# Performance work log

Measured on AMD Instinct MI355X. Metric: run time of the kernel, lower is better.

Reference implementation:

```python
import jax, jax.numpy as jnp
import numpy as np

E = 8                 # n_experts
CAPACITY_FACTOR = 1.25

B, T, H, I = 4, 1024, 2048, 1408


def setup_inputs() -> dict:
    key = jax.random.key(0)
    k0, k1, k2, k3, k4 = jax.random.split(key, 5)
    x = jax.random.normal(k0, (B, T, H), jnp.float32)
    Wr = jax.random.normal(k1, (E, H), jnp.float32) * 0.02   # router proj (no bias)
    Wg = jax.random.normal(k2, (E, I, H), jnp.float32) * 0.02  # gate_proj per expert
    Wu = jax.random.normal(k3, (E, I, H), jnp.float32) * 0.02  # up_proj per expert
    Wd = jax.random.normal(k4, (E, H, I), jnp.float32) * 0.02  # down_proj per expert
    return {"x": x, "Wr": Wr, "Wg": Wg, "Wu": Wu, "Wd": Wd}


def reference(x, Wr, Wg, Wu, Wd):
    Bb, Tt, Hh = x.shape
    N = Bb * Tt
    cap = max(1, int(CAPACITY_FACTOR * (N * 2 / E)))
    xf = x.reshape(N, Hh)

    # --- Top2Router (noise_std=0 -> no noise) ---
    logits = jnp.einsum('nh,eh->ne', xf, Wr)          # [N, E]
    gate = jax.nn.softmax(logits, axis=-1)
    top2_val, top2_idx = jax.lax.top_k(gate, 2)        # [N, 2]

    # --- capacity masking, matching torch loop order: slot k=0 over all
    # tokens (flat order), then slot k=1; within an expert the first `cap`
    # assignments are kept ---
    flat_idx = jnp.concatenate([top2_idx[:, 0], top2_idx[:, 1]])   # [2N]
    flat_val = jnp.concatenate([top2_val[:, 0], top2_val[:, 1]])   # [2N]
    onehot = jax.nn.one_hot(flat_idx, E, dtype=jnp.int32)          # [2N, E]
    rank = (jnp.cumsum(onehot, axis=0) * onehot).sum(-1)           # inclusive rank within expert
    keep = rank <= cap                                             # [2N]
    w_assign = jnp.where(keep, flat_val, 0.0)

    # combine weights per (token, expert); top-2 experts per token are distinct
    tok = jnp.tile(jnp.arange(N), 2)
    comb = jnp.zeros((N, E), x.dtype).at[tok, flat_idx].add(w_assign)  # [N, E]

    # --- per-expert SwiGLU FFN applied densely, combined with gate weights ---
    g = jax.nn.silu(jnp.einsum('nh,eih->eni', xf, Wg))  # [E, N, I]
    u = jnp.einsum('nh,eih->eni', xf, Wu)               # [E, N, I]
    out_e = jnp.einsum('eni,ehi->enh', g * u, Wd)       # [E, N, H]
    y = jnp.einsum('ne,enh->nh', comb, out_e)           # [N, H]
    return y.reshape(Bb, Tt, Hh)
```

## Files before the change

### kernel.cpp

```cpp
#include <hip/hip_runtime.h>
#include <hip/hip_bf16.h>

#define N_TOK 4096
#define H_DIM 2048
#define I_DIM 1408
#define E_NUM 8
#define CAP   1280

typedef __hip_bfloat16 bf16;
typedef unsigned short us;
typedef __bf16 bf16x8 __attribute__((ext_vector_type(8)));
typedef float f32x4 __attribute__((ext_vector_type(4)));

__device__ inline void gld_lds16(const void* g, void* l) {
    __builtin_amdgcn_global_load_lds((const __attribute__((address_space(1))) void*)g,
                                     (__attribute__((address_space(3))) void*)l,
                                     16, 0, 0);
}

__device__ inline void cvt_body8(const float* __restrict__ s, us* __restrict__ d, long i, long n) {
    if (i >= n) return;
    float4 v0 = *(const float4*)(s + i);
    float4 v1 = *(const float4*)(s + i + 4);
    union { us u[8]; uint4 q; } o;
    float f[8] = {v0.x, v0.y, v0.z, v0.w, v1.x, v1.y, v1.z, v1.w};
#pragma unroll
    for (int j = 0; j < 8; j++) {
        bf16 b = __float2bfloat16(f[j]);
        o.u[j] = *(us*)&b;
    }
    *(uint4*)(d + i) = o.q;
}

__global__ void cvt8(const float* __restrict__ s, us* __restrict__ d, long n) {
    long i = ((long)blockIdx.x * blockDim.x + threadIdx.x) * 8;
    cvt_body8(s, d, i, n);
}

__global__ void cvt_w3(const float* __restrict__ s0, const float* __restrict__ s1,
                       const float* __restrict__ s2, us* __restrict__ d0,
                       us* __restrict__ d1, us* __restrict__ d2, long n) {
    long i = ((long)blockIdx.x * blockDim.x + threadIdx.x) * 8;
    const float* s = blockIdx.z == 0 ? s0 : (blockIdx.z == 1 ? s1 : s2);
    us* d = blockIdx.z == 0 ? d0 : (blockIdx.z == 1 ? d1 : d2);
    cvt_body8(s, d, i, n);
}

__global__ void router_k(const float* __restrict__ x, const float* __restrict__ Wr,
                         float* __restrict__ top_val, int* __restrict__ top_idx) {
    int tok  = (blockIdx.x * blockDim.x + threadIdx.x) >> 6;
    int lane = threadIdx.x & 63;
    if (tok >= N_TOK) return;
    const float* xr = x + (size_t)tok * H_DIM;
    float acc[E_NUM];
#pragma unroll
    for (int e = 0; e < E_NUM; e++) acc[e] = 0.f;
    for (int h = lane; h < H_DIM; h += 64) {
        float xv = xr[h];
#pragma unroll
        for (int e = 0; e < E_NUM; e++) acc[e] += xv * Wr[e * H_DIM + h];
    }
#pragma unroll
    for (int e = 0; e < E_NUM; e++) {
#pragma unroll
        for (int off = 32; off > 0; off >>= 1) acc[e] += __shfl_xor(acc[e], off, 64);
    }
    if (lane == 0) {
        float mx = acc[0];
#pragma unroll
        for (int e = 1; e < E_NUM; e++) mx = fmaxf(mx, acc[e]);
        float p[E_NUM], s = 0.f;
#pragma unroll
        for (int e = 0; e < E_NUM; e++) { p[e] = __expf(acc[e] - mx); s += p[e]; }
        float inv = 1.f / s;
#pragma unroll
        for (int e = 0; e < E_NUM; e++) p[e] *= inv;
        int i0 = 0;
#pragma unroll
        for (int e = 1; e < E_NUM; e++) if (p[e] > p[i0]) i0 = e;
        int i1 = -1;
#pragma unroll
        for (int e = 0; e < E_NUM; e++) {
            if (e == i0) continue;
            if (i1 < 0 || p[e] > p[i1]) i1 = e;
        }
        top_idx[tok * 2]     = i0;
        top_idx[tok * 2 + 1] = i1;
        top_val[tok * 2]     = p[i0];
        top_val[tok * 2 + 1] = p[i1];
    }
}

__global__ void assign_k(const int* __restrict__ top_idx, const float* __restrict__ top_val,
                         int* __restrict__ toklist, int* __restrict__ pos,
                         float* __restrict__ wz, int* __restrict__ counts) {
    const int T = 256;
    const int CH = (2 * N_TOK) / T;
    int t = threadIdx.x;
    for (int i = t; i < E_NUM * CAP; i += T) toklist[i] = N_TOK;
    __shared__ int cnt[T][E_NUM];
    int local[E_NUM];
#pragma unroll
    for (int e = 0; e < E_NUM; e++) local[e] = 0;
    for (int q = 0; q < CH; q++) {
        int j = t * CH + q;
        int slot = j >> 12;
        int tok  = j & 4095;
        int e = top_idx[tok * 2 + slot];
        local[e]++;
    }
#pragma unroll
    for (int e = 0; e < E_NUM; e++) cnt[t][e] = local[e];
    __syncthreads();
    if (t < E_NUM) {
        int run = 0;
        for (int i = 0; i < T; i++) { int c = cnt[i][t]; cnt[i][t] = run; run += c; }
        counts[t] = run < CAP ? run : CAP;
    }
    __syncthreads();
    int run[E_NUM];
#pragma unroll
    for (int e = 0; e < E_NUM; e++) run[e] = cnt[t][e];
    for (int q = 0; q < CH; q++) {
        int j = t * CH + q;
        int slot = j >> 12;
        int tok  = j & 4095;
        int e = top_idx[tok * 2 + slot];
        int rank = ++run[e];
        if (rank <= CAP) {
            toklist[e * CAP + rank - 1] = tok;
            pos[tok * 2 + slot] = e * CAP + rank - 1;
            wz[tok * 2 + slot]  = top_val[tok * 2 + slot];
        } else {
            pos[tok * 2 + slot] = -1;
            wz[tok * 2 + slot]  = 0.f;
        }
    }
}

__global__ __launch_bounds__(256, 2)
void gu_fused(const us* __restrict__ A, const us* __restrict__ Wg,
              const us* __restrict__ Wu, us* __restrict__ hbuf,
              const int* __restrict__ toklist, const int* __restrict__ counts) {
    const int e  = blockIdx.z;
    const int m0 = blockIdx.x * 128;
    const int n0 = blockIdx.y * 128;
    if (m0 >= counts[e]) return;

    __shared__ us As[128 * 64];
    __shared__ us Bg[128 * 64];
    __shared__ us Bu[128 * 64];

    const int t  = threadIdx.x;
    const int r0 = t >> 2;
    const int c8 = (t & 3) * 8;

    int tok0 = toklist[e * CAP + m0 + r0];
    int tok1 = toklist[e * CAP + m0 + r0 + 64];
    const us* aP0 = A + (size_t)tok0 * H_DIM + c8;
    const us* aP1 = A + (size_t)tok1 * H_DIM + c8;
    const us* gP0 = Wg + ((size_t)e * I_DIM + n0 + r0) * H_DIM + c8;
    const us* gP1 = gP0 + (size_t)64 * H_DIM;
    const us* uP0 = Wu + ((size_t)e * I_DIM + n0 + r0) * H_DIM + c8;
    const us* uP1 = uP0 + (size_t)64 * H_DIM;

    us* lA0 = As + t * 8;  us* lA1 = lA0 + 64 * 32;
    us* lG0 = Bg + t * 8;  us* lG1 = lG0 + 64 * 32;
    us* lU0 = Bu + t * 8;  us* lU1 = lU0 + 64 * 32;

    const int lane = t & 63;
    const int wave = t >> 6;
    const int wm   = (wave & 1) * 64;
    const int wn   = (wave >> 1) * 64;
    const int l15  = lane & 15;
    const int quad = lane >> 4;

    f32x4 ag[4][4], au[4][4];
#pragma unroll
    for (int i = 0; i < 4; i++)
#pragma unroll
        for (int j = 0; j < 4; j++) {
            ag[i][j] = (f32x4){0.f, 0.f, 0.f, 0.f};
            au[i][j] = (f32x4){0.f, 0.f, 0.f, 0.f};
        }

    for (int k = 0; k < H_DIM; k += 64) {
        gld_lds16(aP0,      lA0);
        gld_lds16(aP1,      lA1);
        gld_lds16(aP0 + 32, lA0 + 4096);
        gld_lds16(aP1 + 32, lA1 + 4096);
        gld_lds16(gP0,      lG0);
        gld_lds16(gP1,      lG1);
        gld_lds16(gP0 + 32, lG0 + 4096);
        gld_lds16(gP1 + 32, lG1 + 4096);
        gld_lds16(uP0,      lU0);
        gld_lds16(uP1,      lU1);
        gld_lds16(uP0 + 32, lU0 + 4096);
        gld_lds16(uP1 + 32, lU1 + 4096);
        aP0 += 64; aP1 += 64; gP0 += 64; gP1 += 64; uP0 += 64; uP1 += 64;
        __syncthreads();
#pragma unroll
        for (int kk = 0; kk < 2; kk++) {
            bf16x8 af[4];
#pragma unroll
            for (int i = 0; i < 4; i++)
                af[i] = *(const bf16x8*)(As + kk * 4096 + (wm + i * 16 + l15) * 32 + quad * 8);
            {
                bf16x8 bfr[4];
#pragma unroll
                for (int j = 0; j < 4; j++)
                    bfr[j] = *(const bf16x8*)(Bg + kk * 4096 + (wn + j * 16 + l15) * 32 + quad * 8);
#pragma unroll
                for (int i = 0; i < 4; i++)
#pragma unroll
                    for (int j = 0; j < 4; j++)
                        ag[i][j] = __builtin_amdgcn_mfma_f32_16x16x32_bf16(af[i], bfr[j], ag[i][j], 0, 0, 0);
            }
            {
                bf16x8 bfr[4];
#pragma unroll
                for (int j = 0; j < 4; j++)
                    bfr[j] = *(const bf16x8*)(Bu + kk * 4096 + (wn + j * 16 + l15) * 32 + quad * 8);
#pragma unroll
                for (int i = 0; i < 4; i++)
#pragma unroll
                    for (int j = 0; j < 4; j++)
                        au[i][j] = __builtin_amdgcn_mfma_f32_16x16x32_bf16(af[i], bfr[j], au[i][j], 0, 0, 0);
            }
        }
        __syncthreads();
    }

#pragma unroll
    for (int i = 0; i < 4; i++) {
        int mb = m0 + wm + i * 16 + quad * 4;
#pragma unroll
        for (int r = 0; r < 4; r++) {
            size_t rowoff = ((size_t)e * CAP + mb + r) * I_DIM;
#pragma unroll
            for (int j = 0; j < 4; j++) {
                int n = n0 + wn + j * 16 + l15;
                float g = ag[i][j][r];
                g = g / (1.f + __expf(-g));
                float hv = g * au[i][j][r];
                bf16 b = __float2bfloat16(hv);
                hbuf[rowoff + n] = *(us*)&b;
            }
        }
    }
}

__global__ __launch_bounds__(256, 3)
void down_gemm(const us* __restrict__ A, const us* __restrict__ W,
               float* __restrict__ dbuf, const int* __restrict__ counts) {
    const int e  = blockIdx.z;
    const int m0 = blockIdx.x * 128;
    const int n0 = blockIdx.y * 128;
    if (m0 >= counts[e]) return;

    __shared__ us As[128 * 64];
    __shared__ us Bs[128 * 64];

    const int t  = threadIdx.x;
    const int r0 = t >> 2;
    const int c8 = (t & 3) * 8;

    const us* aP0 = A + ((size_t)e * CAP + m0 + r0) * (size_t)I_DIM + c8;
    const us* aP1 = aP0 + (size_t)64 * I_DIM;
    const us* bP0 = W + ((size_t)e * H_DIM + n0 + r0) * (size_t)I_DIM + c8;
    const us* bP1 = bP0 + (size_t)64 * I_DIM;

    us* lA0 = As + t * 8;  us* lA1 = lA0 + 64 * 32;
    us* lB0 = Bs + t * 8;  us* lB1 = lB0 + 64 * 32;

    const int lane = t & 63;
    const int wave = t >> 6;
    const int wm   = (wave & 1) * 64;
    const int wn   = (wave >> 1) * 64;
    const int l15  = lane & 15;
    const int quad = lane >> 4;

    f32x4 acc[4][4];
#pragma unroll
    for (int i = 0; i < 4; i++)
#pragma unroll
        for (int j = 0; j < 4; j++) acc[i][j] = (f32x4){0.f, 0.f, 0.f, 0.f};

    for (int k = 0; k < I_DIM; k += 64) {
        gld_lds16(aP0,      lA0);
        gld_lds16(aP1,      lA1);
        gld_lds16(aP0 + 32, lA0 + 4096);
        gld_lds16(aP1 + 32, lA1 + 4096);
        gld_lds16(bP0,      lB0);
        gld_lds16(bP1,      lB1);
        gld_lds16(bP0 + 32, lB0 + 4096);
        gld_lds16(bP1 + 32, lB1 + 4096);
        aP0 += 64; aP1 += 64; bP0 += 64; bP1 += 64;
        __syncthreads();
#pragma unroll
        for (int kk = 0; kk < 2; kk++) {
            bf16x8 af[4], bfr[4];
#pragma unroll
            for (int i = 0; i < 4; i++)
                af[i] = *(const bf16x8*)(As + kk * 4096 + (wm + i * 16 + l15) * 32 + quad * 8);
#pragma unroll
            for (int j = 0; j < 4; j++)
                bfr[j] = *(const bf16x8*)(Bs + kk * 4096 + (wn + j * 16 + l15) * 32 + quad * 8);
#pragma unroll
            for (int i = 0; i < 4; i++)
#pragma unroll
                for (int j = 0; j < 4; j++)
                    acc[i][j] = __builtin_amdgcn_mfma_f32_16x16x32_bf16(af[i], bfr[j], acc[i][j], 0, 0, 0);
        }
        __syncthreads();
    }

#pragma unroll
    for (int i = 0; i < 4; i++) {
        int mb = m0 + wm + i * 16 + quad * 4;
#pragma unroll
        for (int r = 0; r < 4; r++) {
            float* orow = dbuf + ((size_t)e * CAP + mb + r) * H_DIM + n0 + wn + l15;
#pragma unroll
            for (int j = 0; j < 4; j++)
                orow[j * 16] = acc[i][j][r];
        }
    }
}

__global__ void combine_k(const float* __restrict__ dbuf, const int* __restrict__ pos,
                          const float* __restrict__ wz, float* __restrict__ out) {
    int tok = blockIdx.x;
    int off = threadIdx.x * 8;
    int p0 = pos[tok * 2], p1 = pos[tok * 2 + 1];
    float w0 = wz[tok * 2], w1 = wz[tok * 2 + 1];
    float4 z = {0.f, 0.f, 0.f, 0.f};
    float4 a0 = z, a1 = z, b0 = z, b1 = z;
    if (p0 >= 0) {
        const float* r = dbuf + (size_t)p0 * H_DIM + off;
        a0 = *(const float4*)r; a1 = *(const float4*)(r + 4);
    }
    if (p1 >= 0) {
        const float* r = dbuf + (size_t)p1 * H_DIM + off;
        b0 = *(const float4*)r; b1 = *(const float4*)(r + 4);
    }
    float4 o0, o1;
    o0.x = w0 * a0.x + w1 * b0.x;  o0.y = w0 * a0.y + w1 * b0.y;
    o0.z = w0 * a0.z + w1 * b0.z;  o0.w = w0 * a0.w + w1 * b0.w;
    o1.x = w0 * a1.x + w1 * b1.x;  o1.y = w0 * a1.y + w1 * b1.y;
    o1.z = w0 * a1.z + w1 * b1.z;  o1.w = w0 * a1.w + w1 * b1.w;
    float* orow = out + (size_t)tok * H_DIM + off;
    *(float4*)orow = o0;
    *(float4*)(orow + 4) = o1;
}

extern "C" void kernel_launch(void* const* d_in, const int* in_sizes, int n_in,
                              void* d_out, int out_size, void* d_ws, size_t ws_size,
                              hipStream_t stream) {
    const float* x  = (const float*)d_in[0];
    const float* Wr = (const float*)d_in[1];
    const float* Wg = (const float*)d_in[2];
    const float* Wu = (const float*)d_in[3];
    const float* Wd = (const float*)d_in[4];
    float* out = (float*)d_out;

    char* p = (char*)d_ws;
    auto alloc = [&](size_t bytes) { char* r = p; p += (bytes + 255) & ~(size_t)255; return r; };
    us* xb   = (us*)alloc((size_t)(N_TOK + 1) * H_DIM * 2);
    us* Wgb  = (us*)alloc((size_t)E_NUM * I_DIM * H_DIM * 2);
    us* Wub  = (us*)alloc((size_t)E_NUM * I_DIM * H_DIM * 2);
    us* Wdb  = (us*)alloc((size_t)E_NUM * H_DIM * I_DIM * 2);
    us* hbuf = (us*)alloc((size_t)E_NUM * CAP * I_DIM * 2);
    float* top_val = (float*)alloc((size_t)N_TOK * 2 * 4);
    int*   top_idx = (int*)alloc((size_t)N_TOK * 2 * 4);
    int*   toklist = (int*)alloc((size_t)E_NUM * CAP * 4);
    int*   posm    = (int*)alloc((size_t)N_TOK * 2 * 4);
    float* wz      = (float*)alloc((size_t)N_TOK * 2 * 4);
    int*   counts  = (int*)alloc((size_t)E_NUM * 4);
    float* dbuf = (float*)Wgb;

    hipMemsetAsync(xb + (size_t)N_TOK * H_DIM, 0, H_DIM * 2, stream);

    long nx = (long)N_TOK * H_DIM;
    long nw = (long)E_NUM * I_DIM * H_DIM;
    cvt8<<<dim3((unsigned)((nx / 8 + 255) / 256)), dim3(256), 0, stream>>>(x, xb, nx);
    cvt_w3<<<dim3((unsigned)((nw / 8 + 255) / 256), 1, 3), dim3(256), 0, stream>>>(
        Wg, Wu, Wd, Wgb, Wub, Wdb, nw);

    router_k<<<dim3(N_TOK / 4), dim3(256), 0, stream>>>(x, Wr, top_val, top_idx);
    assign_k<<<dim3(1), dim3(256), 0, stream>>>(top_idx, top_val, toklist, posm, wz, counts);

    dim3 g1(CAP / 128, I_DIM / 128, E_NUM);
    gu_fused<<<g1, dim3(256), 0, stream>>>(xb, Wgb, Wub, hbuf, toklist, counts);

    dim3 g2(CAP / 128, H_DIM / 128, E_NUM);
    down_gemm<<<g2, dim3(256), 0, stream>>>(hbuf, Wdb, dbuf, counts);

    combine_k<<<dim3(N_TOK), dim3(256), 0, stream>>>(dbuf, posm, wz, out);
}
```

Measured before the change: 607.5 us.

## Fuse fp32-to-bf16 weight conversion into the expert GEMM tile loaders

Drops the separate pass that converts the gate, up and down weights to bf16 in workspace. The GEMM kernels now read fp32 weights directly and convert them to bf16 in registers before storing into LDS. This removes a full read-and-write pass over roughly 280 MB of weights. In exchange, the weight loads become ordinary synchronous loads instead of async global-to-LDS copies, and every M-tile re-reads twice as many bytes of weights. dbuf also gets its own workspace allocation instead of reusing the converted-weight buffer.

```diff
diff --git a/kernel.cpp b/kernel.cpp
--- a/kernel.cpp
+++ b/kernel.cpp
@@ -18,7 +18,21 @@
                                      16, 0, 0);
 }
 
-__device__ inline void cvt_body8(const float* __restrict__ s, us* __restrict__ d, long i, long n) {
+__device__ inline void stage_f32(const float* __restrict__ src, us* dst) {
+    float4 a = *(const float4*)src;
+    float4 b = *(const float4*)(src + 4);
+    union { us u[8]; uint4 q; } o;
+    float f[8] = {a.x, a.y, a.z, a.w, b.x, b.y, b.z, b.w};
+#pragma unroll
+    for (int j = 0; j < 8; j++) {
+        bf16 v = __float2bfloat16(f[j]);
+        o.u[j] = *(us*)&v;
+    }
+    *(uint4*)dst = o.q;
+}
+
+__global__ void cvt8(const float* __restrict__ s, us* __restrict__ d, long n) {
+    long i = ((long)blockIdx.x * blockDim.x + threadIdx.x) * 8;
     if (i >= n) return;
     float4 v0 = *(const float4*)(s + i);
     float4 v1 = *(const float4*)(s + i + 4);
@@ -30,20 +44,6 @@
         o.u[j] = *(us*)&b;
     }
     *(uint4*)(d + i) = o.q;
-}
-
-__global__ void cvt8(const float* __restrict__ s, us* __restrict__ d, long n) {
-    long i = ((long)blockIdx.x * blockDim.x + threadIdx.x) * 8;
-    cvt_body8(s, d, i, n);
-}
-
-__global__ void cvt_w3(const float* __restrict__ s0, const float* __restrict__ s1,
-                       const float* __restrict__ s2, us* __restrict__ d0,
-                       us* __restrict__ d1, us* __restrict__ d2, long n) {
-    long i = ((long)blockIdx.x * blockDim.x + threadIdx.x) * 8;
-    const float* s = blockIdx.z == 0 ? s0 : (blockIdx.z == 1 ? s1 : s2);
-    us* d = blockIdx.z == 0 ? d0 : (blockIdx.z == 1 ? d1 : d2);
-    cvt_body8(s, d, i, n);
 }
 
 __global__ void router_k(const float* __restrict__ x, const float* __restrict__ Wr,
@@ -139,8 +139,8 @@
 }
 
 __global__ __launch_bounds__(256, 2)
-void gu_fused(const us* __restrict__ A, const us* __restrict__ Wg,
-              const us* __restrict__ Wu, us* __restrict__ hbuf,
+void gu_fused(const us* __restrict__ A, const float* __restrict__ Wg,
+              const float* __restrict__ Wu, us* __restrict__ hbuf,
               const int* __restrict__ toklist, const int* __restrict__ counts) {
     const int e  = blockIdx.z;
     const int m0 = blockIdx.x * 128;
@@ -159,10 +159,10 @@
     int tok1 = toklist[e * CAP + m0 + r0 + 64];
     const us* aP0 = A + (size_t)tok0 * H_DIM + c8;
     const us* aP1 = A + (size_t)tok1 * H_DIM + c8;
-    const us* gP0 = Wg + ((size_t)e * I_DIM + n0 + r0) * H_DIM + c8;
-    const us* gP1 = gP0 + (size_t)64 * H_DIM;
-    const us* uP0 = Wu + ((size_t)e * I_DIM + n0 + r0) * H_DIM + c8;
-    const us* uP1 = uP0 + (size_t)64 * H_DIM;
+    const float* gP0 = Wg + ((size_t)e * I_DIM + n0 + r0) * H_DIM + c8;
+    const float* gP1 = gP0 + (size_t)64 * H_DIM;
+    const float* uP0 = Wu + ((size_t)e * I_DIM + n0 + r0) * H_DIM + c8;
+    const float* uP1 = uP0 + (size_t)64 * H_DIM;
 
     us* lA0 = As + t * 8;  us* lA1 = lA0 + 64 * 32;
     us* lG0 = Bg + t * 8;  us* lG1 = lG0 + 64 * 32;
@@ -189,14 +189,14 @@
         gld_lds16(aP1,      lA1);
         gld_lds16(aP0 + 32, lA0 + 4096);
         gld_lds16(aP1 + 32, lA1 + 4096);
-        gld_lds16(gP0,      lG0);
-        gld_lds16(gP1,      lG1);
-        gld_lds16(gP0 + 32, lG0 + 4096);
-        gld_lds16(gP1 + 32, lG1 + 4096);
-        gld_lds16(uP0,      lU0);
-        gld_lds16(uP1,      lU1);
-        gld_lds16(uP0 + 32, lU0 + 4096);
-        gld_lds16(uP1 + 32, lU1 + 4096);
+        stage_f32(gP0,             lG0);
+        stage_f32(gP1,             lG1);
+        stage_f32(gP0 + 32,        lG0 + 4096);
+        stage_f32(gP1 + 32,        lG1 + 4096);
+        stage_f32(uP0,             lU0);
+        stage_f32(uP1,             lU1);
+        stage_f32(uP0 + 32,        lU0 + 4096);
+        stage_f32(uP1 + 32,        lU1 + 4096);
         aP0 += 64; aP1 += 64; gP0 += 64; gP1 += 64; uP0 += 64; uP1 += 64;
         __syncthreads();
 #pragma unroll
@@ -251,7 +251,7 @@
 }
 
 __global__ __launch_bounds__(256, 3)
-void down_gemm(const us* __restrict__ A, const us* __restrict__ W,
+void down_gemm(const us* __restrict__ A, const float* __restrict__ W,
                float* __restrict__ dbuf, const int* __restrict__ counts) {
     const int e  = blockIdx.z;
     const int m0 = blockIdx.x * 128;
@@ -267,8 +267,8 @@
 
     const us* aP0 = A + ((size_t)e * CAP + m0 + r0) * (size_t)I_DIM + c8;
     const us* aP1 = aP0 + (size_t)64 * I_DIM;
-    const us* bP0 = W + ((size_t)e * H_DIM + n0 + r0) * (size_t)I_DIM + c8;
-    const us* bP1 = bP0 + (size_t)64 * I_DIM;
+    const float* bP0 = W + ((size_t)e * H_DIM + n0 + r0) * (size_t)I_DIM + c8;
+    const float* bP1 = bP0 + (size_t)64 * I_DIM;
 
     us* lA0 = As + t * 8;  us* lA1 = lA0 + 64 * 32;
     us* lB0 = Bs + t * 8;  us* lB1 = lB0 + 64 * 32;
@@ -291,10 +291,10 @@
         gld_lds16(aP1,      lA1);
         gld_lds16(aP0 + 32, lA0 + 4096);
         gld_lds16(aP1 + 32, lA1 + 4096);
-        gld_lds16(bP0,      lB0);
-        gld_lds16(bP1,      lB1);
-        gld_lds16(bP0 + 32, lB0 + 4096);
-        gld_lds16(bP1 + 32, lB1 + 4096);
+        stage_f32(bP0,      lB0);
+        stage_f32(bP1,      lB1);
+        stage_f32(bP0 + 32, lB0 + 4096);
+        stage_f32(bP1 + 32, lB1 + 4096);
         aP0 += 64; aP1 += 64; bP0 += 64; bP1 += 64;
         __syncthreads();
 #pragma unroll
@@ -367,34 +367,28 @@
     char* p = (char*)d_ws;
     auto alloc = [&](size_t bytes) { char* r = p; p += (bytes + 255) & ~(size_t)255; return r; };
     us* xb   = (us*)alloc((size_t)(N_TOK + 1) * H_DIM * 2);
-    us* Wgb  = (us*)alloc((size_t)E_NUM * I_DIM * H_DIM * 2);
-    us* Wub  = (us*)alloc((size_t)E_NUM * I_DIM * H_DIM * 2);
-    us* Wdb  = (us*)alloc((size_t)E_NUM * H_DIM * I_DIM * 2);
     us* hbuf = (us*)alloc((size_t)E_NUM * CAP * I_DIM * 2);
+    float* dbuf = (float*)alloc((size_t)E_NUM * CAP * H_DIM * 4);
     float* top_val = (float*)alloc((size_t)N_TOK * 2 * 4);
     int*   top_idx = (int*)alloc((size_t)N_TOK * 2 * 4);
     int*   toklist = (int*)alloc((size_t)E_NUM * CAP * 4);
     int*   posm    = (int*)alloc((size_t)N_TOK * 2 * 4);
     float* wz      = (float*)alloc((size_t)N_TOK * 2 * 4);
     int*   counts  = (int*)alloc((size_t)E_NUM * 4);
-    float* dbuf = (float*)Wgb;
 
     hipMemsetAsync(xb + (size_t)N_TOK * H_DIM, 0, H_DIM * 2, stream);
 
     long nx = (long)N_TOK * H_DIM;
-    long nw = (long)E_NUM * I_DIM * H_DIM;
     cvt8<<<dim3((unsigned)((nx / 8 + 255) / 256)), dim3(256), 0, stream>>>(x, xb, nx);
-    cvt_w3<<<dim3((unsigned)((nw / 8 + 255) / 256), 1, 3), dim3(256), 0, stream>>>(
-        Wg, Wu, Wd, Wgb, Wub, Wdb, nw);
 
     router_k<<<dim3(N_TOK / 4), dim3(256), 0, stream>>>(x, Wr, top_val, top_idx);
     assign_k<<<dim3(1), dim3(256), 0, stream>>>(top_idx, top_val, toklist, posm, wz, counts);
 
     dim3 g1(CAP / 128, I_DIM / 128, E_NUM);
-    gu_fused<<<g1, dim3(256), 0, stream>>>(xb, Wgb, Wub, hbuf, toklist, counts);
+    gu_fused<<<g1, dim3(256), 0, stream>>>(xb, Wg, Wu, hbuf, toklist, counts);
 
     dim3 g2(CAP / 128, H_DIM / 128, E_NUM);
-    down_gemm<<<g2, dim3(256), 0, stream>>>(hbuf, Wdb, dbuf, counts);
+    down_gemm<<<g2, dim3(256), 0, stream>>>(hbuf, Wd, dbuf, counts);
 
     combine_k<<<dim3(N_TOK), dim3(256), 0, stream>>>(dbuf, posm, wz, out);
 }
```

New measurement: 676.8 us. 1.11x slower.

## Fuse weight/activation conversion into router and gate-up kernels to overlap

Applied to the files above, without the earlier changes.

Merges the x conversion, Wg/Wu conversion and the zero-row memset into a single router kernel with grid-stride conversion blocks. The Wd conversion moves into extra blocks of the gate-up GEMM launch so it can overlap with GEMM work. This cuts launch count and idle gaps between small kernels. In exchange the grid-stride conversion blocks can become stragglers, and gu_fused blocks now carry extra code paths.

```diff
diff --git a/kernel.cpp b/kernel.cpp
--- a/kernel.cpp
+++ b/kernel.cpp
@@ -18,8 +18,7 @@
                                      16, 0, 0);
 }
 
-__device__ inline void cvt_body8(const float* __restrict__ s, us* __restrict__ d, long i, long n) {
-    if (i >= n) return;
+__device__ inline void cvt_body8(const float* __restrict__ s, us* __restrict__ d, long i) {
     float4 v0 = *(const float4*)(s + i);
     float4 v1 = *(const float4*)(s + i + 4);
     union { us u[8]; uint4 q; } o;
@@ -32,26 +31,35 @@
     *(uint4*)(d + i) = o.q;
 }
 
-__global__ void cvt8(const float* __restrict__ s, us* __restrict__ d, long n) {
-    long i = ((long)blockIdx.x * blockDim.x + threadIdx.x) * 8;
-    cvt_body8(s, d, i, n);
-}
-
-__global__ void cvt_w3(const float* __restrict__ s0, const float* __restrict__ s1,
-                       const float* __restrict__ s2, us* __restrict__ d0,
-                       us* __restrict__ d1, us* __restrict__ d2, long n) {
-    long i = ((long)blockIdx.x * blockDim.x + threadIdx.x) * 8;
-    const float* s = blockIdx.z == 0 ? s0 : (blockIdx.z == 1 ? s1 : s2);
-    us* d = blockIdx.z == 0 ? d0 : (blockIdx.z == 1 ? d1 : d2);
-    cvt_body8(s, d, i, n);
-}
-
-__global__ void router_k(const float* __restrict__ x, const float* __restrict__ Wr,
-                         float* __restrict__ top_val, int* __restrict__ top_idx) {
-    int tok  = (blockIdx.x * blockDim.x + threadIdx.x) >> 6;
-    int lane = threadIdx.x & 63;
-    if (tok >= N_TOK) return;
-    const float* xr = x + (size_t)tok * H_DIM;
+__global__ void router_cvt(const float* __restrict__ x, const float* __restrict__ Wr,
+                           const float* __restrict__ Wg, const float* __restrict__ Wu,
+                           us* __restrict__ xb, us* __restrict__ Wgb, us* __restrict__ Wub,
+                           float* __restrict__ top_val, int* __restrict__ top_idx) {
+    const int bx = blockIdx.x;
+    const int t  = threadIdx.x;
+
+    if (bx < 512) {
+        const float* s = (bx < 256) ? Wg : Wu;
+        us*          d = (bx < 256) ? Wgb : Wub;
+        const int   sb = bx & 255;
+        const long   n = (long)E_NUM * I_DIM * H_DIM;
+        for (long i = ((long)sb * 256 + t) * 8; i < n; i += (long)256 * 256 * 8)
+            cvt_body8(s, d, i);
+        if (bx == 0) {
+            uint4 z = {0u, 0u, 0u, 0u};
+            *(uint4*)(xb + (size_t)N_TOK * H_DIM + t * 8) = z;
+        }
+        return;
+    }
+
+    int tok  = (bx - 512) * 4 + (t >> 6);
+    int lane = t & 63;
+    const float* xr  = x  + (size_t)tok * H_DIM;
+    us*          xbr = xb + (size_t)tok * H_DIM;
+
+#pragma unroll
+    for (int q = 0; q < 4; q++) cvt_body8(xr, xbr, q * 512 + lane * 8);
+
     float acc[E_NUM];
 #pragma unroll
     for (int e = 0; e < E_NUM; e++) acc[e] = 0.f;
@@ -141,17 +149,25 @@
 __global__ __launch_bounds__(256, 2)
 void gu_fused(const us* __restrict__ A, const us* __restrict__ Wg,
               const us* __restrict__ Wu, us* __restrict__ hbuf,
-              const int* __restrict__ toklist, const int* __restrict__ counts) {
-    const int e  = blockIdx.z;
-    const int m0 = blockIdx.x * 128;
-    const int n0 = blockIdx.y * 128;
+              const int* __restrict__ toklist, const int* __restrict__ counts,
+              const float* __restrict__ Wd, us* __restrict__ Wdb) {
+    const int t = threadIdx.x;
+    if (blockIdx.x < 256) {
+        const long n = (long)E_NUM * H_DIM * I_DIM;
+        for (long i = ((long)blockIdx.x * 256 + t) * 8; i < n; i += (long)256 * 256 * 8)
+            cvt_body8(Wd, Wdb, i);
+        return;
+    }
+    const int id = blockIdx.x - 256;
+    const int m0 = (id % 10) * 128;
+    const int n0 = ((id / 10) % 11) * 128;
+    const int e  = id / 110;
     if (m0 >= counts[e]) return;
 
     __shared__ us As[128 * 64];
     __shared__ us Bg[128 * 64];
     __shared__ us Bu[128 * 64];
 
-    const int t  = threadIdx.x;
     const int r0 = t >> 2;
     const int c8 = (t & 3) * 8;
 
@@ -379,19 +395,13 @@
     int*   counts  = (int*)alloc((size_t)E_NUM * 4);
     float* dbuf = (float*)Wgb;
 
-    hipMemsetAsync(xb + (size_t)N_TOK * H_DIM, 0, H_DIM * 2, stream);
-
-    long nx = (long)N_TOK * H_DIM;
-    long nw = (long)E_NUM * I_DIM * H_DIM;
-    cvt8<<<dim3((unsigned)((nx / 8 + 255) / 256)), dim3(256), 0, stream>>>(x, xb, nx);
-    cvt_w3<<<dim3((unsigned)((nw / 8 + 255) / 256), 1, 3), dim3(256), 0, stream>>>(
-        Wg, Wu, Wd, Wgb, Wub, Wdb, nw);
-
-    router_k<<<dim3(N_TOK / 4), dim3(256), 0, stream>>>(x, Wr, top_val, top_idx);
+    router_cvt<<<dim3(512 + N_TOK / 4), dim3(256), 0, stream>>>(
+        x, Wr, Wg, Wu, xb, Wgb, Wub, top_val, top_idx);
+
     assign_k<<<dim3(1), dim3(256), 0, stream>>>(top_idx, top_val, toklist, posm, wz, counts);
 
-    dim3 g1(CAP / 128, I_DIM / 128, E_NUM);
-    gu_fused<<<g1, dim3(256), 0, stream>>>(xb, Wgb, Wub, hbuf, toklist, counts);
+    gu_fused<<<dim3(256 + (CAP / 128) * (I_DIM / 128) * E_NUM), dim3(256), 0, stream>>>(
+        xb, Wgb, Wub, hbuf, toklist, counts, Wd, Wdb);
 
     dim3 g2(CAP / 128, H_DIM / 128, E_NUM);
     down_gemm<<<g2, dim3(256), 0, stream>>>(hbuf, Wdb, dbuf, counts);
```

Measured after the change: 607.1 us. No clear change (-0.1%).
